# Kernel tuning notes

Hardware: AMD Instinct MI355X
Metric: run time of the kernel (lower is better)

Reference implementation:

```python
import jax, jax.numpy as jnp
import numpy as np

N = 1024          # num_nodes
E = 16384         # num_edges (avg degree 16)
D = 256           # in_channels
P = 2.0           # PairwiseDistance p
SELF_ADD = 0.5
UPPER_BOUND = 2.0
# scores lie in [SELF_ADD, 1+SELF_ADD] = [0.5, 1.5], so the greedy loop adds
# at most ceil(UPPER_BOUND / 0.5) = 4 edges; 6 masked steps is a safe bound.
MAX_STEPS = 6


def setup_inputs() -> dict:
    key = jax.random.key(0)
    k1, k2 = jax.random.split(key)
    x = jax.random.normal(k1, (N, D), dtype=jnp.float32)
    edge_index = jax.random.randint(k2, (2, E), 0, N, dtype=jnp.int64)
    return {"x": x, "edge_index": edge_index}


def _edge_scores(x, src, dst):
    # compute_distance_score: L2 pairwise distance, min-max normalized, + self_add
    diff = x[src] - x[dst]                      # [E, D]
    dist = jnp.sqrt(jnp.sum(diff * diff, axis=-1))
    dist = (dist - dist.min()) / (dist.max() - dist.min())
    return dist + SELF_ADD                      # [E]


def _search_all(edge_score, src, dst):
    # Vectorized version of node__cluster_search: for each seed node i, greedily
    # add the min-score edge leaving the cluster until total score >= UPPER_BOUND
    # or no frontier edge exists. Fixed-length masked scan == original while-loop.
    def search(i):
        inc = jnp.zeros((N,), bool).at[i].set(True)      # in_cluster mask
        row = jnp.zeros((N,), jnp.float32)               # node_score_matrix row
        tot = jnp.float32(0.0)

        def step(state, _):
            inc, row, tot = state
            valid = inc[src] & ~inc[dst]                 # frontier edges [E]
            active = (tot < UPPER_BOUND) & jnp.any(valid)
            masked = jnp.where(valid, edge_score, jnp.inf)
            e = jnp.argmin(masked)                       # min-score frontier edge
            s = edge_score[e]
            u, v = src[e], dst[e]
            inc2 = inc.at[v].set(True)
            row2 = row.at[u].add(s * 0.5).at[v].add(s * 0.5)
            inc = jnp.where(active, inc2, inc)
            row = jnp.where(active, row2, row)
            tot = jnp.where(active, tot + s, tot)
            return (inc, row, tot), None

        (inc, row, tot), _ = jax.lax.scan(step, (inc, row, tot), None, length=MAX_STEPS)
        return inc.astype(jnp.float32), row

    return jax.vmap(search)(jnp.arange(N))


def _keep_first_unique_rows(assign):
    # np.unique(..., axis=0) dedup, shape-static variant: keep first occurrence of
    # each distinct binary row, zero out duplicates. Double random-hash row compare.
    rng = np.random.default_rng(12345)
    r1 = jnp.asarray(rng.integers(1, 2**20, size=(N,)), dtype=jnp.int32)
    r2 = jnp.asarray(rng.integers(1, 2**20, size=(N,)), dtype=jnp.int32)
    ai = assign.astype(jnp.int32)
    h1, h2 = ai @ r1, ai @ r2
    eq = (h1[:, None] == h1[None, :]) & (h2[:, None] == h2[None, :])  # [N, N]
    dup = jnp.any(jnp.tril(eq, k=-1), axis=1)
    return (~dup).astype(jnp.float32)


def reference(x, edge_index):
    src, dst = edge_index[0], edge_index[1]
    edge_score = _edge_scores(x, src, dst)
    assign, nsm = _search_all(edge_score, src, dst)      # [N, N], [N, N]

    keep = _keep_first_unique_rows(assign)               # [N]
    assign_k = assign * keep[:, None]
    nsm_k = nsm * keep[:, None]

    # dense adjacency (to_dense_adj), pooled adjacency, binarize, drop self-loops
    adj = jnp.zeros((N, N), jnp.float32).at[src, dst].add(1.0)
    adj_new = assign_k @ adj @ assign_k.T
    adj_new = (adj_new > 0).astype(jnp.float32) * (1.0 - jnp.eye(N, dtype=jnp.float32))

    x_new = nsm_k @ x                                    # pooled features [N, D]
    return adj_new, x_new, assign_k, nsm_k
```

## Files before the change

### kernel.cpp

```cpp
#include <hip/hip_runtime.h>
#include <cstdint>

#define NN 1024
#define NE 16384
#define DF 256
#define UB 2.0f
#define MAXSEL 6
#define CAP 64
#define NB2 1024
#define DSTR 16
#define FILLB 176

typedef unsigned long long u64;

__global__ void k_fill(uint4* __restrict__ p) {
    uint32_t v = (blockIdx.x < 128) ? 0xFFFFFFFFu : 0u;
    p[blockIdx.x * 256 + threadIdx.x] = make_uint4(v, v, v, v);
}

__global__ void k_dist_build(const float* __restrict__ x, const int* __restrict__ src,
                             const int* __restrict__ dst, int* __restrict__ deg,
                             u64* __restrict__ slots,
                             uint32_t* __restrict__ pmin, uint32_t* __restrict__ pmax) {
    __shared__ uint32_t smin[4], smax[4];
    int t = threadIdx.x;
    int wid = t >> 6, lane = t & 63;
    int c16 = lane & 15;
    int e = blockIdx.x * 16 + wid * 4 + (lane >> 4);
    int u = src[e], v = dst[e];
    const float4* xa = (const float4*)(x + (size_t)u * DF);
    const float4* xb = (const float4*)(x + (size_t)v * DF);
    float4 a0 = xa[c16],      b0 = xb[c16];
    float4 a1 = xa[c16 + 16], b1 = xb[c16 + 16];
    float4 a2 = xa[c16 + 32], b2 = xb[c16 + 32];
    float4 a3 = xa[c16 + 48], b3 = xb[c16 + 48];
    double s = 0.0;
    {
        float d;
        d = a0.x-b0.x; s += (double)d*d;  d = a0.y-b0.y; s += (double)d*d;
        d = a0.z-b0.z; s += (double)d*d;  d = a0.w-b0.w; s += (double)d*d;
        d = a1.x-b1.x; s += (double)d*d;  d = a1.y-b1.y; s += (double)d*d;
        d = a1.z-b1.z; s += (double)d*d;  d = a1.w-b1.w; s += (double)d*d;
        d = a2.x-b2.x; s += (double)d*d;  d = a2.y-b2.y; s += (double)d*d;
        d = a2.z-b2.z; s += (double)d*d;  d = a2.w-b2.w; s += (double)d*d;
        d = a3.x-b3.x; s += (double)d*d;  d = a3.y-b3.y; s += (double)d*d;
        d = a3.z-b3.z; s += (double)d*d;  d = a3.w-b3.w; s += (double)d*d;
    }
    s += __shfl_xor(s, 1, 64);
    s += __shfl_xor(s, 2, 64);
    s += __shfl_xor(s, 4, 64);
    s += __shfl_xor(s, 8, 64);
    uint32_t db = __float_as_uint(sqrtf((float)s));
    if (c16 == 0) {
        int pos = atomicAdd(&deg[u * DSTR], 1);
        if (pos < CAP)
            slots[(size_t)u * CAP + pos] =
                ((u64)db << 24) | ((u64)(uint32_t)e << 10) | (u64)(uint32_t)v;
    }
    uint32_t mnv = db, mxv = db;
    uint32_t o;
    o = (uint32_t)__shfl_xor((int)mnv, 16, 64); mnv = min(mnv, o);
    o = (uint32_t)__shfl_xor((int)mnv, 32, 64); mnv = min(mnv, o);
    o = (uint32_t)__shfl_xor((int)mxv, 16, 64); mxv = max(mxv, o);
    o = (uint32_t)__shfl_xor((int)mxv, 32, 64); mxv = max(mxv, o);
    if (lane == 0) { smin[wid] = mnv; smax[wid] = mxv; }
    __syncthreads();
    if (t == 0) {
        pmin[blockIdx.x] = min(min(smin[0], smin[1]), min(smin[2], smin[3]));
        pmax[blockIdx.x] = max(max(smax[0], smax[1]), max(smax[2], smax[3]));
    }
}

__global__ void k_search(const u64* __restrict__ slots,
                         const uint32_t* __restrict__ pmin, const uint32_t* __restrict__ pmax,
                         const int* __restrict__ src,
                         uint32_t* __restrict__ masks, uint32_t* __restrict__ maskT,
                         int* __restrict__ selU, int* __restrict__ selV,
                         float* __restrict__ selS, int* __restrict__ selCnt,
                         u64* __restrict__ sig, u64* __restrict__ dc64) {
    __shared__ u64 pool[8][64];
    __shared__ uint32_t inc[32];
    __shared__ int members[8];
    __shared__ float s_tot;
    __shared__ int s_nmem;
    int i = blockIdx.x, lane = threadIdx.x;
    if (lane < 32) inc[lane] = 0;

    uint32_t mnb = 0xFFFFFFFFu, mxb = 0u;
    const uint4* p4n = (const uint4*)pmin;
    const uint4* p4x = (const uint4*)pmax;
    for (int k = lane; k < NB2 / 4; k += 64) {
        uint4 a = p4n[k], b = p4x[k];
        mnb = min(mnb, min(min(a.x, a.y), min(a.z, a.w)));
        mxb = max(mxb, max(max(b.x, b.y), max(b.z, b.w)));
    }
    for (int off = 32; off; off >>= 1) {
        uint32_t oa = (uint32_t)__shfl_xor((int)mnb, off, 64);
        uint32_t ob = (uint32_t)__shfl_xor((int)mxb, off, 64);
        mnb = min(mnb, oa);
        mxb = max(mxb, ob);
    }
    float MN = __uint_as_float(mnb);
    float MX = __uint_as_float(mxb);

    if (lane == 0) {
        inc[i >> 5] = 1u << (i & 31);
        members[0] = i;
        s_tot = 0.0f;
        s_nmem = 1;
    }
    pool[0][lane] = slots[(size_t)i * CAP + lane];
    __syncthreads();
    int cnt = 0;
    for (int step = 0; step < MAXSEL; ++step) {
        if (s_tot >= UB) break;
        int nm = s_nmem;
        u64 best = ~0ull;
        #pragma unroll
        for (int m = 0; m < 8; ++m) {
            if (m < nm) {
                u64 en = pool[m][lane];
                int v = (int)(en & 1023);
                if (!((inc[v >> 5] >> (v & 31)) & 1u) && en < best) best = en;
            }
        }
        for (int off = 32; off; off >>= 1) {
            u64 o = __shfl_xor(best, off, 64);
            if (o < best) best = o;
        }
        if (best == ~0ull) break;
        if (lane == 0) {
            uint32_t db = (uint32_t)(best >> 24);
            int e = (int)((best >> 10) & 0x3FFF);
            int v = (int)(best & 1023);
            float dd = __uint_as_float(db);
            float s = (dd - MN) / (MX - MN) + 0.5f;
            inc[v >> 5] |= 1u << (v & 31);
            members[s_nmem++] = v;
            selU[i * 8 + cnt] = src[e];
            selV[i * 8 + cnt] = v;
            selS[i * 8 + cnt] = s;
            s_tot += s;
        }
        cnt++;
        __syncthreads();
        int newm = s_nmem - 1;
        pool[newm][lane] = slots[(size_t)members[newm] * CAP + lane];
        __syncthreads();
    }
    __syncthreads();
    if (lane == 0) {
        selCnt[i] = cnt;
        u64 h = 1469598103934665603ull;
        for (int w = 0; w < 32; ++w) { h ^= inc[w]; h *= 1099511628211ull; }
        sig[i] = h;
        u64 d = 0; int nc = 0;
        for (int k = 1; k < s_nmem; ++k) {
            int v = members[k];
            if (v < i) { d |= ((u64)(uint32_t)v) << (4 + 10 * nc); ++nc; }
        }
        dc64[i] = d | (u64)nc;
    }
    if (lane < 32) masks[(size_t)i * 32 + lane] = inc[lane];
    if (lane < s_nmem) {
        int n = members[lane];
        atomicOr(&maskT[(size_t)n * 32 + (i >> 5)], 1u << (i & 31));
    }
}

__global__ void k_rows(const float* __restrict__ x, const u64* __restrict__ slots,
                       const uint32_t* __restrict__ masks, const uint32_t* __restrict__ maskT,
                       const u64* __restrict__ sig, const u64* __restrict__ dc64,
                       const int* __restrict__ selU, const int* __restrict__ selV,
                       const float* __restrict__ selS, const int* __restrict__ selCnt,
                       float* __restrict__ outAdj, float* __restrict__ outAs,
                       float* __restrict__ outNsm, float* __restrict__ outX) {
    __shared__ u64 sigL[NN];
    __shared__ uint32_t keepb[32];
    __shared__ uint32_t R[32], MI[32], orow[32];
    __shared__ uint32_t part[8][32];
    __shared__ int list[512];
    __shared__ int s_lcnt;
    __shared__ int su[8], ssv[8];
    __shared__ float ss[8];
    __shared__ int s_c;
    int i = blockIdx.x, t = threadIdx.x;

    for (int j = t; j < NN; j += 256) sigL[j] = sig[j];
    if (t < 32) { keepb[t] = 0; R[t] = 0; MI[t] = masks[(size_t)i * 32 + t]; }
    if (t == 0) { s_c = selCnt[i]; s_lcnt = 0; }
    if (t < 8) { su[t] = selU[i*8+t]; ssv[t] = selV[i*8+t]; ss[t] = selS[i*8+t]; }
    __syncthreads();

    for (int q = 0; q < 4; ++q) {
        int j = t + q * 256;
        u64 d = dc64[j];
        int cj = (int)(d & 15);
        u64 sj = sigL[j];
        bool dup = false;
        for (int k = 0; k < cj; ++k) {
            int v = (int)((d >> (4 + 10 * k)) & 1023);
            if (sigL[v] == sj) { dup = true; break; }
        }
        if (!dup) atomicOr(&keepb[j >> 5], 1u << (j & 31));
    }

    int c = s_c;
    int total = (c + 1) * CAP;
    for (int k = t; k < total; k += 256) {
        int m = k >> 6;
        int u = (m == 0) ? i : ssv[m - 1];
        u64 en = slots[(size_t)u * CAP + (k & 63)];
        if (en != ~0ull) {
            int v = (int)(en & 1023);
            atomicOr(&R[v >> 5], 1u << (v & 31));
        }
    }
    __syncthreads();
    int kp = (keepb[i >> 5] >> (i & 31)) & 1;

    if (t < 32) {
        uint32_t bits = R[t];
        while (bits) {
            int b = __ffs(bits) - 1;
            bits &= bits - 1;
            int p = atomicAdd(&s_lcnt, 1);
            list[p] = t * 32 + b;
        }
    }
    __syncthreads();
    int lcnt = s_lcnt;

    int g = t >> 5, l = t & 31;
    uint32_t acc = 0;
    if (kp) {
        for (int k = g; k < lcnt; k += 8)
            acc |= maskT[(size_t)list[k] * 32 + l];
    }
    part[g][l] = acc;
    __syncthreads();
    if (t < 32) {
        uint32_t o = 0;
        for (int gg = 0; gg < 8; ++gg) o |= part[gg][t];
        orow[t] = o & keepb[t];
    }
    __syncthreads();

    int j0 = t * 4;
    int w = j0 >> 5, sh = j0 & 31;
    float4 vadj = {0,0,0,0}, vas = {0,0,0,0}, vnsm = {0,0,0,0};
    if (kp) {
        uint32_t ob = orow[w] >> sh;
        uint32_t mb = MI[w] >> sh;
        vadj.x = ((ob     ) & 1) && (j0     != i) ? 1.0f : 0.0f;
        vadj.y = ((ob >> 1) & 1) && (j0 + 1 != i) ? 1.0f : 0.0f;
        vadj.z = ((ob >> 2) & 1) && (j0 + 2 != i) ? 1.0f : 0.0f;
        vadj.w = ((ob >> 3) & 1) && (j0 + 3 != i) ? 1.0f : 0.0f;
        vas.x = (mb      & 1) ? 1.0f : 0.0f;
        vas.y = ((mb>>1) & 1) ? 1.0f : 0.0f;
        vas.z = ((mb>>2) & 1) ? 1.0f : 0.0f;
        vas.w = ((mb>>3) & 1) ? 1.0f : 0.0f;
        for (int k = 0; k < c; ++k) {
            float h = ss[k] * 0.5f;
            int u = su[k], v = ssv[k];
            vnsm.x += ((u == j0    ) ? h : 0.0f) + ((v == j0    ) ? h : 0.0f);
            vnsm.y += ((u == j0 + 1) ? h : 0.0f) + ((v == j0 + 1) ? h : 0.0f);
            vnsm.z += ((u == j0 + 2) ? h : 0.0f) + ((v == j0 + 2) ? h : 0.0f);
            vnsm.w += ((u == j0 + 3) ? h : 0.0f) + ((v == j0 + 3) ? h : 0.0f);
        }
    }
    ((float4*)outAdj)[(size_t)i * (NN/4) + t] = vadj;
    ((float4*)outAs )[(size_t)i * (NN/4) + t] = vas;
    ((float4*)outNsm)[(size_t)i * (NN/4) + t] = vnsm;

    float accx = 0.0f;
    if (kp) {
        for (int k = 0; k < c; ++k) {
            float h = ss[k] * 0.5f;
            accx += h * x[(size_t)su[k] * DF + t];
            accx += h * x[(size_t)ssv[k] * DF + t];
        }
    }
    outX[(size_t)i * DF + t] = accx;
}

extern "C" void kernel_launch(void* const* d_in, const int* in_sizes, int n_in,
                              void* d_out, int out_size, void* d_ws, size_t ws_size,
                              hipStream_t stream) {
    const float* x = (const float*)d_in[0];
    const int* ei = (const int*)d_in[1];
    const int* src = ei;
    const int* dst = ei + NE;

    float* out = (float*)d_out;
    float* out_adj = out;
    float* out_x   = out + (size_t)NN * NN;
    float* out_as  = out_x + (size_t)NN * DF;
    float* out_nsm = out_as + (size_t)NN * NN;

    char* w = (char*)d_ws;
    u64*      slots = (u64*)w;       w += (size_t)NN * CAP * 8;
    int*      deg   = (int*)w;       w += (size_t)NN * DSTR * 4;
    uint32_t* maskT = (uint32_t*)w;  w += (size_t)NN * 32 * 4;
    u64*      sig   = (u64*)w;       w += (size_t)NN * 8;
    u64*      dc64  = (u64*)w;       w += (size_t)NN * 8;
    uint32_t* pmin  = (uint32_t*)w;  w += (size_t)NB2 * 4;
    uint32_t* pmax  = (uint32_t*)w;  w += (size_t)NB2 * 4;
    uint32_t* masks = (uint32_t*)w;  w += (size_t)NN * 32 * 4;
    int*      selU  = (int*)w;       w += (size_t)NN * 8 * 4;
    int*      selV  = (int*)w;       w += (size_t)NN * 8 * 4;
    float*    selS  = (float*)w;     w += (size_t)NN * 8 * 4;
    int*      selCnt= (int*)w;       w += (size_t)NN * 4;

    k_fill<<<FILLB, 256, 0, stream>>>((uint4*)slots);
    k_dist_build<<<NB2, 256, 0, stream>>>(x, src, dst, deg, slots, pmin, pmax);
    k_search<<<NN, 64, 0, stream>>>(slots, pmin, pmax, src,
                                    masks, maskT, selU, selV, selS, selCnt, sig, dc64);
    k_rows<<<NN, 256, 0, stream>>>(x, slots, masks, maskT, sig, dc64,
                                   selU, selV, selS, selCnt,
                                   out_adj, out_as, out_nsm, out_x);
}
```

Measured before the change: 33.77 us.

## Drop slot prefill, bound adjacency slots by degree, and cut shared-state syncs

The slot array is no longer pre-filled with sentinels. Only the degree and maskT region is zeroed, and readers now bound valid slots by the per-node degree count. The search kernel keeps the total and member count in registers and reads the newly added node's slots before the barrier, removing one __syncthreads per step. The row-list build in k_rows uses a warp prefix scan instead of shared atomics. The workspace is reordered so one small zero kernel covers deg and maskT. Correctness depends on the zeroed span exactly matching deg plus maskT.

```diff
diff --git a/kernel.cpp b/kernel.cpp
--- a/kernel.cpp
+++ b/kernel.cpp
@@ -9,13 +9,11 @@
 #define CAP 64
 #define NB2 1024
 #define DSTR 16
-#define FILLB 176
 
 typedef unsigned long long u64;
 
-__global__ void k_fill(uint4* __restrict__ p) {
-    uint32_t v = (blockIdx.x < 128) ? 0xFFFFFFFFu : 0u;
-    p[blockIdx.x * 256 + threadIdx.x] = make_uint4(v, v, v, v);
+__global__ void k_zero(uint4* __restrict__ p) {
+    p[blockIdx.x * 256 + threadIdx.x] = make_uint4(0, 0, 0, 0);
 }
 
 __global__ void k_dist_build(const float* __restrict__ x, const int* __restrict__ src,
@@ -71,7 +69,7 @@
     }
 }
 
-__global__ void k_search(const u64* __restrict__ slots,
+__global__ void k_search(const int* __restrict__ deg, const u64* __restrict__ slots,
                          const uint32_t* __restrict__ pmin, const uint32_t* __restrict__ pmax,
                          const int* __restrict__ src,
                          uint32_t* __restrict__ masks, uint32_t* __restrict__ maskT,
@@ -81,8 +79,6 @@
     __shared__ u64 pool[8][64];
     __shared__ uint32_t inc[32];
     __shared__ int members[8];
-    __shared__ float s_tot;
-    __shared__ int s_nmem;
     int i = blockIdx.x, lane = threadIdx.x;
     if (lane < 32) inc[lane] = 0;
 
@@ -103,22 +99,20 @@
     float MN = __uint_as_float(mnb);
     float MX = __uint_as_float(mxb);
 
-    if (lane == 0) {
-        inc[i >> 5] = 1u << (i & 31);
-        members[0] = i;
-        s_tot = 0.0f;
-        s_nmem = 1;
-    }
-    pool[0][lane] = slots[(size_t)i * CAP + lane];
-    __syncthreads();
-    int cnt = 0;
+    int dv0 = deg[i * DSTR];
+    u64 g0 = slots[(size_t)i * CAP + lane];
+    if (lane == 0) { inc[i >> 5] = 1u << (i & 31); members[0] = i; }
+    pool[0][lane] = (lane < min(dv0, CAP)) ? g0 : ~0ull;
+    float tot = 0.0f;
+    int nmem = 1, cnt = 0;
+    __syncthreads();
+
     for (int step = 0; step < MAXSEL; ++step) {
-        if (s_tot >= UB) break;
-        int nm = s_nmem;
+        if (tot >= UB) break;
         u64 best = ~0ull;
         #pragma unroll
         for (int m = 0; m < 8; ++m) {
-            if (m < nm) {
+            if (m < nmem) {
                 u64 en = pool[m][lane];
                 int v = (int)(en & 1023);
                 if (!((inc[v >> 5] >> (v & 31)) & 1u) && en < best) best = en;
@@ -129,23 +123,22 @@
             if (o < best) best = o;
         }
         if (best == ~0ull) break;
+        uint32_t db = (uint32_t)(best >> 24);
+        int e = (int)((best >> 10) & 0x3FFF);
+        int v = (int)(best & 1023);
+        float s = (__uint_as_float(db) - MN) / (MX - MN) + 0.5f;
+        int dvn = deg[v * DSTR];
+        u64 gn = slots[(size_t)v * CAP + lane];
         if (lane == 0) {
-            uint32_t db = (uint32_t)(best >> 24);
-            int e = (int)((best >> 10) & 0x3FFF);
-            int v = (int)(best & 1023);
-            float dd = __uint_as_float(db);
-            float s = (dd - MN) / (MX - MN) + 0.5f;
             inc[v >> 5] |= 1u << (v & 31);
-            members[s_nmem++] = v;
+            members[nmem] = v;
             selU[i * 8 + cnt] = src[e];
             selV[i * 8 + cnt] = v;
             selS[i * 8 + cnt] = s;
-            s_tot += s;
-        }
-        cnt++;
-        __syncthreads();
-        int newm = s_nmem - 1;
-        pool[newm][lane] = slots[(size_t)members[newm] * CAP + lane];
+        }
+        pool[nmem][lane] = (lane < min(dvn, CAP)) ? gn : ~0ull;
+        tot += s;
+        nmem++; cnt++;
         __syncthreads();
     }
     __syncthreads();
@@ -155,20 +148,21 @@
         for (int w = 0; w < 32; ++w) { h ^= inc[w]; h *= 1099511628211ull; }
         sig[i] = h;
         u64 d = 0; int nc = 0;
-        for (int k = 1; k < s_nmem; ++k) {
+        for (int k = 1; k < nmem; ++k) {
             int v = members[k];
             if (v < i) { d |= ((u64)(uint32_t)v) << (4 + 10 * nc); ++nc; }
         }
         dc64[i] = d | (u64)nc;
     }
     if (lane < 32) masks[(size_t)i * 32 + lane] = inc[lane];
-    if (lane < s_nmem) {
+    if (lane < nmem) {
         int n = members[lane];
         atomicOr(&maskT[(size_t)n * 32 + (i >> 5)], 1u << (i & 31));
     }
 }
 
-__global__ void k_rows(const float* __restrict__ x, const u64* __restrict__ slots,
+__global__ void k_rows(const float* __restrict__ x, const int* __restrict__ deg,
+                       const u64* __restrict__ slots,
                        const uint32_t* __restrict__ masks, const uint32_t* __restrict__ maskT,
                        const u64* __restrict__ sig, const u64* __restrict__ dc64,
                        const int* __restrict__ selU, const int* __restrict__ selV,
@@ -188,7 +182,7 @@
 
     for (int j = t; j < NN; j += 256) sigL[j] = sig[j];
     if (t < 32) { keepb[t] = 0; R[t] = 0; MI[t] = masks[(size_t)i * 32 + t]; }
-    if (t == 0) { s_c = selCnt[i]; s_lcnt = 0; }
+    if (t == 0) s_c = selCnt[i];
     if (t < 8) { su[t] = selU[i*8+t]; ssv[t] = selV[i*8+t]; ss[t] = selS[i*8+t]; }
     __syncthreads();
 
@@ -210,8 +204,9 @@
     for (int k = t; k < total; k += 256) {
         int m = k >> 6;
         int u = (m == 0) ? i : ssv[m - 1];
+        int dv = min(deg[u * DSTR], CAP);
         u64 en = slots[(size_t)u * CAP + (k & 63)];
-        if (en != ~0ull) {
+        if ((k & 63) < dv) {
             int v = (int)(en & 1023);
             atomicOr(&R[v >> 5], 1u << (v & 31));
         }
@@ -219,14 +214,24 @@
     __syncthreads();
     int kp = (keepb[i >> 5] >> (i & 31)) & 1;
 
-    if (t < 32) {
-        uint32_t bits = R[t];
-        while (bits) {
-            int b = __ffs(bits) - 1;
-            bits &= bits - 1;
-            int p = atomicAdd(&s_lcnt, 1);
-            list[p] = t * 32 + b;
-        }
+    if (t < 64) {
+        uint32_t bits = (t < 32) ? R[t] : 0u;
+        int pc = __popc(bits);
+        int inc_scan = pc;
+        #pragma unroll
+        for (int d = 1; d < 64; d <<= 1) {
+            int o = __shfl_up(inc_scan, d, 64);
+            if (t >= d) inc_scan += o;
+        }
+        int off = inc_scan - pc;
+        if (t < 32) {
+            while (bits) {
+                int b = __ffs(bits) - 1;
+                bits &= bits - 1;
+                list[off++] = t * 32 + b;
+            }
+        }
+        if (t == 31) s_lcnt = inc_scan;
     }
     __syncthreads();
     int lcnt = s_lcnt;
@@ -300,10 +305,10 @@
 
     char* w = (char*)d_ws;
     u64*      slots = (u64*)w;       w += (size_t)NN * CAP * 8;
+    u64*      sig   = (u64*)w;       w += (size_t)NN * 8;
+    u64*      dc64  = (u64*)w;       w += (size_t)NN * 8;
     int*      deg   = (int*)w;       w += (size_t)NN * DSTR * 4;
     uint32_t* maskT = (uint32_t*)w;  w += (size_t)NN * 32 * 4;
-    u64*      sig   = (u64*)w;       w += (size_t)NN * 8;
-    u64*      dc64  = (u64*)w;       w += (size_t)NN * 8;
     uint32_t* pmin  = (uint32_t*)w;  w += (size_t)NB2 * 4;
     uint32_t* pmax  = (uint32_t*)w;  w += (size_t)NB2 * 4;
     uint32_t* masks = (uint32_t*)w;  w += (size_t)NN * 32 * 4;
@@ -312,11 +317,11 @@
     float*    selS  = (float*)w;     w += (size_t)NN * 8 * 4;
     int*      selCnt= (int*)w;       w += (size_t)NN * 4;
 
-    k_fill<<<FILLB, 256, 0, stream>>>((uint4*)slots);
+    k_zero<<<48, 256, 0, stream>>>((uint4*)deg);
     k_dist_build<<<NB2, 256, 0, stream>>>(x, src, dst, deg, slots, pmin, pmax);
-    k_search<<<NN, 64, 0, stream>>>(slots, pmin, pmax, src,
+    k_search<<<NN, 64, 0, stream>>>(deg, slots, pmin, pmax, src,
                                     masks, maskT, selU, selV, selS, selCnt, sig, dc64);
-    k_rows<<<NN, 256, 0, stream>>>(x, slots, masks, maskT, sig, dc64,
+    k_rows<<<NN, 256, 0, stream>>>(x, deg, slots, masks, maskT, sig, dc64,
                                    selU, selV, selS, selCnt,
                                    out_adj, out_as, out_nsm, out_x);
 }
```

Result: no change. 33.68 us (-0.3%).
